# Performance work log

Hardware: AMD Instinct MI355X
Metric: run time of the kernel (lower is better)

The kernel has to match this reference:

```python
import jax, jax.numpy as jnp
import numpy as np

B, N, C, H = 4, 1025, 768, 12
KEEP_RATIO = 0.25
BETA = 1.0


def setup_inputs() -> dict:
    key = jax.random.key(0)
    k1, k2, k3, k4, k5 = jax.random.split(key, 5)
    x = jax.random.normal(k1, (B, N, C), dtype=jnp.float32)
    ucb_count_score = jax.random.uniform(k2, (H, N), dtype=jnp.float32)
    W_qkv = jax.random.normal(k3, (C, 3 * C), dtype=jnp.float32) * 0.02
    W_proj = jax.random.normal(k4, (C, C), dtype=jnp.float32) * 0.02
    b_proj = jax.random.normal(k5, (C,), dtype=jnp.float32) * 0.02
    return {"x": x, "ucb_count_score": ucb_count_score, "W_qkv": W_qkv,
            "W_proj": W_proj, "b_proj": b_proj, "counter": 100, "ucb_enabled": 1}


def reference(x, ucb_count_score, W_qkv, W_proj, b_proj, counter, ucb_enabled):
    Bn, Nn, Cn = x.shape
    Dh = Cn // H
    scale = Dh ** -0.5
    # qkv projection (no bias, qkv_bias=False)
    qkv = (x @ W_qkv).reshape(Bn, Nn, 3, H, Dh)
    q = jnp.transpose(qkv[:, :, 0], (0, 2, 1, 3))  # [B,H,N,Dh]
    k = jnp.transpose(qkv[:, :, 1], (0, 2, 1, 3))
    v = jnp.transpose(qkv[:, :, 2], (0, 2, 1, 3))
    attn_probs = jax.nn.softmax(jnp.einsum('bhnd,bhmd->bhnm', q, k) * scale, axis=-1)

    if ucb_enabled and counter > 50:
        # UCB pruning path (exclude_cls=True, keep_ratio set)
        total_patches = Nn - 1
        k_sel = max(1, int(total_patches * KEEP_RATIO))
        patch_scores = attn_probs[:, :, :, 1:].mean(axis=2)  # [B,H,N-1]
        expl = BETA * jnp.sqrt(jnp.log(counter + 1.0) / (ucb_count_score[:, 1:] + 1e-6))  # [H,N-1]
        global_ucb = (patch_scores + expl[None]).mean(axis=1)  # [B,N-1]
        _, sel = jax.lax.top_k(global_ucb, k_sel)  # [B,k]
        tok = sel + 1  # shift for CLS
        # keep[b,j] = 1 if token j is CLS or selected in batch b
        keep = jnp.zeros((Bn, Nn), dtype=attn_probs.dtype)
        keep = keep.at[jnp.arange(Bn)[:, None], tok].set(1.0).at[:, 0].set(1.0)
        # mask[b,h,i,j] = keep[b,i] OR keep[b,j]
        mask = jnp.maximum(keep[:, None, :, None], keep[:, None, None, :])
        pruned = attn_probs * mask
        pruned = pruned / (pruned.sum(axis=-1, keepdims=True) + 1e-8)
        context = jnp.einsum('bhnm,bhmd->bhnd', pruned, v)
        cnt = jnp.zeros((Nn,), dtype=jnp.float32).at[tok.reshape(-1)].add(1.0) / Bn
        score_delta = jnp.broadcast_to(cnt[None, :], ucb_count_score.shape)
    else:
        context = jnp.einsum('bhnm,bhmd->bhnd', attn_probs, v)
        score_delta = None

    out = context.transpose(0, 2, 1, 3).reshape(Bn, Nn, Cn) @ W_proj + b_proj
    return out, score_delta
```

## Files before the change

### kernel.cpp

```cpp
#include <hip/hip_runtime.h>
#include <hip/hip_bf16.h>
#include <math.h>

#define Bb 4
#define Nn 1025
#define Cc 768
#define Hh 12
#define BH (Bb*Hh)
#define M_ROWS 4100
#define KSEL 256
#define JP 1152
#define IT_TILES 68
#define NIB 17
#define NIB32 33
#define NSW 9
#define MT16 264
#define KC24 24
#define JT16 72
#define JS32 36
#define ESTR 1160
#define NPART 396
#define QSCALE 0.18033688011112042f

#define CAST_X_BLK 1584
#define CAST_WQKV_BLK 864
#define CAST_WPROJ_BLK 288

typedef __attribute__((ext_vector_type(8))) short short8;
typedef __attribute__((ext_vector_type(4))) float floatx4;

static __device__ inline unsigned short f2bf(float v) {
    __hip_bfloat16 b = __float2bfloat16(v);
    return *reinterpret_cast<unsigned short*>(&b);
}
static __device__ inline unsigned short tbf(float f) {
    union { float f; unsigned u; } x; x.f = f;
    return (unsigned short)(x.u >> 16);
}
static __device__ inline float fexp2(float x) {
    return __builtin_amdgcn_exp2f(x);
}
static __device__ inline float bflo(unsigned u) {
    return __uint_as_float((u & 0xffffu) << 16);
}
static __device__ inline float bfhi(unsigned u) {
    return __uint_as_float(u & 0xffff0000u);
}

static __device__ inline void async16(const unsigned short* g, unsigned short* l) {
    __builtin_amdgcn_global_load_lds(
        (const __attribute__((address_space(1))) unsigned int*)g,
        (__attribute__((address_space(3))) unsigned int*)l, 16, 0, 0);
}

__global__ __launch_bounds__(256)
void cast_all(const float* __restrict__ x, const float* __restrict__ Wqkv,
              const float* __restrict__ Wproj,
              unsigned short* __restrict__ xA, unsigned short* __restrict__ WB,
              unsigned short* __restrict__ WpB)
{
    int blk = blockIdx.x;
    int tid = threadIdx.x;
    if (blk < CAST_X_BLK) {
        int s = blk * 256 + tid;
        int ml = s & 15, q = (s >> 4) & 3;
        int t2 = s >> 6;
        int mt = t2 % MT16, kc = t2 / MT16;
        int m = mt * 16 + ml, k = kc * 32 + q * 8;
        uint4 pk = {0u, 0u, 0u, 0u};
        if (m < M_ROWS) {
            float4 a = *(const float4*)&x[(size_t)m * 768 + k];
            float4 b2 = *(const float4*)&x[(size_t)m * 768 + k + 4];
            pk.x = (unsigned)f2bf(a.x)  | ((unsigned)f2bf(a.y)  << 16);
            pk.y = (unsigned)f2bf(a.z)  | ((unsigned)f2bf(a.w)  << 16);
            pk.z = (unsigned)f2bf(b2.x) | ((unsigned)f2bf(b2.y) << 16);
            pk.w = (unsigned)f2bf(b2.z) | ((unsigned)f2bf(b2.w) << 16);
        }
        *(uint4*)&xA[(size_t)s * 8] = pk;
        return;
    }
    const float* W;
    unsigned short* WO;
    int N, NT, s;
    if (blk < CAST_X_BLK + CAST_WQKV_BLK) {
        W = Wqkv; WO = WB; N = 2304; NT = 144;
        s = (blk - CAST_X_BLK) * 256 + tid;
    } else {
        W = Wproj; WO = WpB; N = 768; NT = 48;
        s = (blk - CAST_X_BLK - CAST_WQKV_BLK) * 256 + tid;
    }
    int nl = s & 15, q = (s >> 4) & 3;
    int t2 = s >> 6;
    int nt = t2 % NT, kc = t2 / NT;
    int n = nt * 16 + nl, k = kc * 32 + q * 8;
    unsigned hv[8];
#pragma unroll
    for (int e = 0; e < 8; ++e)
        hv[e] = f2bf(W[(size_t)(k + e) * N + n]);
    uint4 pk;
    pk.x = hv[0] | (hv[1] << 16);
    pk.y = hv[2] | (hv[3] << 16);
    pk.z = hv[4] | (hv[5] << 16);
    pk.w = hv[6] | (hv[7] << 16);
    *(uint4*)&WO[(size_t)s * 8] = pk;
}

__global__ __launch_bounds__(256, 2)
void gemm_mfma(const unsigned short* __restrict__ Af,
               const unsigned short* __restrict__ Bf,
               int Nt16, int mode,
               unsigned short* __restrict__ qB, unsigned short* __restrict__ kF,
               unsigned short* __restrict__ vF,
               float* __restrict__ outp, const float* __restrict__ bias)
{
    __shared__ __align__(16) unsigned short ldsA[4096];
    __shared__ __align__(16) unsigned short ldsB[4096];
    const int tid = threadIdx.x;
    const int ln = tid & 63, w = tid >> 6;
    const int wm = w >> 1, wn = w & 1;
    const int mb = blockIdx.x, nb = blockIdx.y;

    floatx4 acc[4][4];
#pragma unroll
    for (int mt = 0; mt < 4; ++mt)
#pragma unroll
        for (int nt = 0; nt < 4; ++nt)
            acc[mt][nt] = (floatx4){0.f, 0.f, 0.f, 0.f};

    for (int kc = 0; kc < KC24; ++kc) {
        const unsigned short* gA = Af + ((size_t)(kc * MT16 + mb * 8)) * 512;
        const unsigned short* gB = Bf + ((size_t)(kc * Nt16 + nb * 8)) * 512;
        async16(gA + (size_t)(w * 128 + ln) * 8,      &ldsA[w * 1024]);
        async16(gA + (size_t)(w * 128 + 64 + ln) * 8, &ldsA[w * 1024 + 512]);
        async16(gB + (size_t)(w * 128 + ln) * 8,      &ldsB[w * 1024]);
        async16(gB + (size_t)(w * 128 + 64 + ln) * 8, &ldsB[w * 1024 + 512]);
        __syncthreads();

        short8 Am[4], Bn[4];
#pragma unroll
        for (int mt = 0; mt < 4; ++mt)
            Am[mt] = *(const short8*)&ldsA[((wm * 4 + mt) * 64 + ln) * 8];
#pragma unroll
        for (int nt = 0; nt < 4; ++nt)
            Bn[nt] = *(const short8*)&ldsB[((wn * 4 + nt) * 64 + ln) * 8];
#pragma unroll
        for (int mt = 0; mt < 4; ++mt)
#pragma unroll
            for (int nt = 0; nt < 4; ++nt)
                acc[mt][nt] = __builtin_amdgcn_mfma_f32_16x16x32_bf16(
                    Am[mt], Bn[nt], acc[mt][nt], 0, 0, 0);
        __syncthreads();
    }

    const int q = ln >> 4, l15 = ln & 15;
    if (mode == 1) {
#pragma unroll
        for (int nt = 0; nt < 4; ++nt) {
            int gn = nb * 128 + wn * 64 + nt * 16 + l15;
            float bv = bias[gn];
#pragma unroll
            for (int mt = 0; mt < 4; ++mt) {
                int gmb = mb * 128 + wm * 64 + mt * 16 + q * 4;
#pragma unroll
                for (int r = 0; r < 4; ++r) {
                    int gm = gmb + r;
                    if (gm < M_ROWS)
                        outp[(size_t)gm * 768 + gn] = acc[mt][nt][r] + bv;
                }
            }
        }
    } else {
#pragma unroll
        for (int nt = 0; nt < 4; ++nt) {
            int gn = nb * 128 + wn * 64 + nt * 16 + l15;
            int s = (gn >= 1536) ? 2 : (gn >= 768 ? 1 : 0);
            int rr = gn - s * Cc;
            int h = rr >> 6, d = rr & 63;
#pragma unroll
            for (int mt = 0; mt < 4; ++mt) {
                int gmb = mb * 128 + wm * 64 + mt * 16 + q * 4;
#pragma unroll
                for (int r = 0; r < 4; ++r) {
                    int gm = gmb + r;
                    if (gm >= M_ROWS) continue;
                    int b = gm / Nn;
                    int n = gm - b * Nn;
                    int bh = b * Hh + h;
                    float val = acc[mt][nt][r];
                    if (s == 0) {
                        int idx = (((bh * IT_TILES + (n >> 4)) * 2 + (d >> 5)) * 512)
                                  + ((((d & 31) >> 3) * 16 + (n & 15)) * 8) + (d & 7);
                        qB[idx] = f2bf(val * QSCALE);
                    } else if (s == 1) {
                        size_t idx = ((((size_t)bh * JT16 + (n >> 4)) * 2 + (d >> 5)) * 64
                                      + ((d >> 3) & 3) * 16 + (n & 15)) * 8 + (d & 7);
                        kF[idx] = f2bf(val);
                    } else {
                        size_t idx = ((((size_t)bh * JS32 + (n >> 5)) * 4 + (d >> 4)) * 64
                                      + ((n >> 3) & 3) * 16 + (d & 15)) * 8 + (n & 7);
                        vF[idx] = f2bf(val);
                    }
                }
            }
        }
    }
}

__global__ __launch_bounds__(256, 2)
void attn_colsum_mfma(const unsigned short* __restrict__ qB,
                      const unsigned short* __restrict__ kF,
                      float* __restrict__ colsum_part)
{
    __shared__ unsigned short expS[32 * ESTR];
    __shared__ float red16[16][32];
    __shared__ float linv[32];

    const int blk = blockIdx.x;
    const int x8 = blk & 7, g = blk >> 3;
    const int bh = x8 * 6 + (g % 6);
    const int ib = g / 6;
    const int tid = threadIdx.x;
    const int ws = tid >> 6;
    const int ln = tid & 63;
    const int i16 = ln & 15, q = ln >> 4;

    const unsigned short* kBase = kF + (size_t)bh * JT16 * 1024;

    short8 Qf[2][2];
#pragma unroll
    for (int it = 0; it < 2; ++it)
#pragma unroll
        for (int kc = 0; kc < 2; ++kc)
            Qf[it][kc] = *(const short8*)&qB[(((size_t)bh * IT_TILES + ib * 2 + it) * 2 + kc) * 512 + ln * 8];

    float lacc[2][2] = {{0.f, 0.f}, {0.f, 0.f}};

    short8 Kc[2][2], Kn[2][2];
#pragma unroll
    for (int jt = 0; jt < 2; ++jt)
#pragma unroll
        for (int kc = 0; kc < 2; ++kc)
            Kc[jt][kc] = *(const short8*)&kBase[(((ws * 2 + jt) * 2 + kc) * 64 + ln) * 8];

    for (int sw = 0; sw < NSW; ++sw) {
        if (sw + 1 < NSW) {
#pragma unroll
            for (int jt = 0; jt < 2; ++jt)
#pragma unroll
                for (int kc = 0; kc < 2; ++kc)
                    Kn[jt][kc] = *(const short8*)&kBase[((((sw + 1) * 8 + ws * 2 + jt) * 2 + kc) * 64 + ln) * 8];
        }

        floatx4 S[2][2];
#pragma unroll
        for (int it = 0; it < 2; ++it)
#pragma unroll
            for (int jt = 0; jt < 2; ++jt) {
                S[it][jt] = (floatx4){0.f, 0.f, 0.f, 0.f};
#pragma unroll
                for (int kc = 0; kc < 2; ++kc)
                    S[it][jt] = __builtin_amdgcn_mfma_f32_16x16x32_bf16(Kc[jt][kc], Qf[it][kc], S[it][jt], 0, 0, 0);
            }

        const int jbase0 = sw * 128 + ws * 32 + q * 4;
#pragma unroll
        for (int it = 0; it < 2; ++it) {
            const int irow = it * 16 + i16;
#pragma unroll
            for (int jt = 0; jt < 2; ++jt) {
                int jbase = jbase0 + jt * 16;
                float p[4];
#pragma unroll
                for (int r = 0; r < 4; ++r) {
                    float vld = (jbase + r < Nn) ? 1.f : 0.f;
                    p[r] = fexp2(S[it][jt][r]) * vld;
                }
                lacc[it][jt] += (p[0] + p[1]) + (p[2] + p[3]);
                uint2 pk;
                pk.x = (unsigned)tbf(p[0]) | ((unsigned)tbf(p[1]) << 16);
                pk.y = (unsigned)tbf(p[2]) | ((unsigned)tbf(p[3]) << 16);
                *(uint2*)&expS[irow * ESTR + jbase] = pk;
            }
        }
#pragma unroll
        for (int jt = 0; jt < 2; ++jt)
#pragma unroll
            for (int kc = 0; kc < 2; ++kc)
                Kc[jt][kc] = Kn[jt][kc];
    }

    __syncthreads();
#pragma unroll
    for (int it = 0; it < 2; ++it)
        red16[ws * 4 + q][it * 16 + i16] = lacc[it][0] + lacc[it][1];
    __syncthreads();
    if (tid < 32) {
        float s = 0.f;
#pragma unroll
        for (int t = 0; t < 16; ++t) s += red16[t][tid];
        int gi = ib * 32 + tid;
        linv[tid] = (gi < Nn) ? 1.f / s : 0.f;
    }
    __syncthreads();

    float* prow = colsum_part + (size_t)(bh * NIB32 + ib) * JP;
    for (int grp = tid; grp < 288; grp += 256) {
        int j0 = grp * 4;
        float a0 = 0.f, a1 = 0.f, a2 = 0.f, a3 = 0.f;
#pragma unroll 8
        for (int i = 0; i < 32; ++i) {
            uint2 v = *(const uint2*)&expS[i * ESTR + j0];
            float li = linv[i];
            a0 += bflo(v.x) * li;
            a1 += bfhi(v.x) * li;
            a2 += bflo(v.y) * li;
            a3 += bfhi(v.y) * li;
        }
        float4 o = {a0, a1, a2, a3};
        *(float4*)&prow[j0] = o;
    }
}

__global__ __launch_bounds__(1024)
void ucb_topk(const float* __restrict__ colsum_part, const float* __restrict__ ucb_score,
              const int* __restrict__ counter_p,
              float* __restrict__ keepP, float* __restrict__ cnt_b)
{
    const int b = blockIdx.x;
    const int tid = threadIdx.x;
    __shared__ float vals[1024];
    __shared__ int   idxs[1024];

    for (int t = tid; t < JP; t += 1024) {
        keepP[b * JP + t] = 0.f;
        cnt_b[b * JP + t] = 0.f;
    }

    const int j = tid + 1;
    const float* pb = colsum_part + (size_t)b * NPART * JP + j;
    float c0 = 0.f, c1 = 0.f, c2 = 0.f, c3 = 0.f;
#pragma unroll 4
    for (int g2 = 0; g2 < NPART; g2 += 4) {
        c0 += pb[(size_t)(g2 + 0) * JP];
        c1 += pb[(size_t)(g2 + 1) * JP];
        c2 += pb[(size_t)(g2 + 2) * JP];
        c3 += pb[(size_t)(g2 + 3) * JP];
    }
    float cs = (c0 + c1) + (c2 + c3);

    float lc = logf((float)(*counter_p) + 1.0f);
    float s = cs * (1.0f / (float)Nn);
#pragma unroll
    for (int h = 0; h < Hh; ++h)
        s += sqrtf(lc / (ucb_score[h * Nn + j] + 1e-6f));
    s *= (1.0f / (float)Hh);
    vals[tid] = s; idxs[tid] = tid;
    __syncthreads();

    for (int k = 2; k <= 1024; k <<= 1) {
        for (int jj = k >> 1; jj > 0; jj >>= 1) {
            int partner = tid ^ jj;
            if (partner > tid) {
                float v1 = vals[tid], v2 = vals[partner];
                int i1 = idxs[tid], i2 = idxs[partner];
                bool gt = (v1 > v2) || (v1 == v2 && i1 < i2);
                bool desc = ((tid & k) == 0);
                if (desc ? !gt : gt) {
                    vals[tid] = v2; vals[partner] = v1;
                    idxs[tid] = i2; idxs[partner] = i1;
                }
            }
            __syncthreads();
        }
    }

    if (tid < KSEL) {
        int tok = idxs[tid] + 1;
        keepP[b * JP + tok] = 1.f;
        cnt_b[b * JP + tok] = 1.0f / (float)Bb;
    }
    if (tid == 0) keepP[b * JP + 0] = 1.f;
}

__global__ __launch_bounds__(256, 2)
void attn_ctx_mfma(const unsigned short* __restrict__ qB,
                   const unsigned short* __restrict__ kF,
                   const unsigned short* __restrict__ vF,
                   const float* __restrict__ keepP, const float* __restrict__ cnt_b,
                   unsigned short* __restrict__ ctxA, float* __restrict__ out2)
{
    __shared__ __align__(16) char smem[29440];
    unsigned short* Pall = (unsigned short*)smem;
    float* red16 = (float*)(smem + 20480);
    float* dinv  = (float*)(smem + 24576);
    float* keeps = (float*)(smem + 24832);
    float* redC  = (float*)smem;

    const int blk = blockIdx.x;
    const int x8 = blk & 7, g = blk >> 3;
    const int bh = x8 * 6 + (g % 6);
    const int ib = g / 6;
    const int b = bh / Hh, h = bh % Hh;
    const int tid = threadIdx.x;
    const int ws = tid >> 6;
    const int ln = tid & 63;
    const int i16 = ln & 15, q = ln >> 4;

    {
        int t = blk * 256 + tid;
        if (t < Hh * Nn) {
            int n = t % Nn;
            out2[t] = cnt_b[0 * JP + n] + cnt_b[1 * JP + n]
                    + cnt_b[2 * JP + n] + cnt_b[3 * JP + n];
        }
    }

    for (int t = tid; t < JP; t += 256) keeps[t] = keepP[b * JP + t];

    const unsigned short* kBase = kF + (size_t)bh * JT16 * 1024;
    const unsigned short* vBase = vF + (size_t)bh * JS32 * 2048;

    short8 Qf[4][2];
#pragma unroll
    for (int it = 0; it < 4; ++it)
#pragma unroll
        for (int kc = 0; kc < 2; ++kc)
            Qf[it][kc] = *(const short8*)&qB[(((size_t)bh * IT_TILES + ib * 4 + it) * 2 + kc) * 512 + ln * 8];

    __syncthreads();

    float keepi[4];
#pragma unroll
    for (int it = 0; it < 4; ++it)
        keepi[it] = keeps[(ib * 4 + it) * 16 + i16];

    floatx4 ctxacc[4][4];
#pragma unroll
    for (int it = 0; it < 4; ++it)
#pragma unroll
        for (int dt = 0; dt < 4; ++dt)
            ctxacc[it][dt] = (floatx4){0.f, 0.f, 0.f, 0.f};
    float dsacc[4] = {0.f, 0.f, 0.f, 0.f};

    unsigned short* Pw = Pall + ws * 2560;

    short8 Kc[2][2], Kn[2][2], Vc[4], Vn[4];
#pragma unroll
    for (int jt = 0; jt < 2; ++jt)
#pragma unroll
        for (int kc = 0; kc < 2; ++kc)
            Kc[jt][kc] = *(const short8*)&kBase[(((ws * 2 + jt) * 2 + kc) * 64 + ln) * 8];
#pragma unroll
    for (int dt = 0; dt < 4; ++dt)
        Vc[dt] = *(const short8*)&vBase[((ws * 4 + dt) * 64 + ln) * 8];

    for (int sw = 0; sw < NSW; ++sw) {
        if (sw + 1 < NSW) {
#pragma unroll
            for (int jt = 0; jt < 2; ++jt)
#pragma unroll
                for (int kc = 0; kc < 2; ++kc)
                    Kn[jt][kc] = *(const short8*)&kBase[((((sw + 1) * 8 + ws * 2 + jt) * 2 + kc) * 64 + ln) * 8];
#pragma unroll
            for (int dt = 0; dt < 4; ++dt)
                Vn[dt] = *(const short8*)&vBase[((((sw + 1) * 4 + ws) * 4 + dt) * 64 + ln) * 8];
        }

        float kjv[2][4], vld[2][4];
#pragma unroll
        for (int jt = 0; jt < 2; ++jt)
#pragma unroll
            for (int r = 0; r < 4; ++r) {
                int jj = sw * 128 + ws * 32 + jt * 16 + q * 4 + r;
                vld[jt][r] = (jj < Nn) ? 1.f : 0.f;
                kjv[jt][r] = keeps[jj];
            }

#pragma unroll
        for (int it = 0; it < 4; ++it) {
            floatx4 S[2];
#pragma unroll
            for (int jt = 0; jt < 2; ++jt) {
                S[jt] = (floatx4){0.f, 0.f, 0.f, 0.f};
#pragma unroll
                for (int kc = 0; kc < 2; ++kc)
                    S[jt] = __builtin_amdgcn_mfma_f32_16x16x32_bf16(Kc[jt][kc], Qf[it][kc], S[jt], 0, 0, 0);
            }
            bool rk = keepi[it] > 0.5f;
#pragma unroll
            for (int jt = 0; jt < 2; ++jt) {
                float p[4];
#pragma unroll
                for (int r = 0; r < 4; ++r) {
                    float w = rk ? vld[jt][r] : kjv[jt][r];
                    p[r] = fexp2(S[jt][r]) * w;
                    dsacc[it] += p[r];
                }
                unsigned int lo = (unsigned)tbf(p[0]) | ((unsigned)tbf(p[1]) << 16);
                unsigned int hi = (unsigned)tbf(p[2]) | ((unsigned)tbf(p[3]) << 16);
                uint2 pk; pk.x = lo; pk.y = hi;
                *(uint2*)&Pw[(it * 16 + i16) * 40 + jt * 16 + q * 4] = pk;
            }
        }

        short8 Pf[4];
#pragma unroll
        for (int it = 0; it < 4; ++it)
            Pf[it] = *(const short8*)&Pw[(it * 16 + i16) * 40 + q * 8];
#pragma unroll
        for (int it = 0; it < 4; ++it)
#pragma unroll
            for (int dt = 0; dt < 4; ++dt)
                ctxacc[it][dt] = __builtin_amdgcn_mfma_f32_16x16x32_bf16(Pf[it], Vc[dt], ctxacc[it][dt], 0, 0, 0);

#pragma unroll
        for (int jt = 0; jt < 2; ++jt)
#pragma unroll
            for (int kc = 0; kc < 2; ++kc)
                Kc[jt][kc] = Kn[jt][kc];
#pragma unroll
        for (int dt = 0; dt < 4; ++dt)
            Vc[dt] = Vn[dt];
    }

    __syncthreads();
#pragma unroll
    for (int it = 0; it < 4; ++it) red16[(ws * 4 + q) * 64 + it * 16 + i16] = dsacc[it];
    __syncthreads();
    if (tid < 64) {
        float s = 0.f;
#pragma unroll
        for (int t = 0; t < 16; ++t) s += red16[t * 64 + tid];
        dinv[tid] = 1.f / (s + 1e-8f);
    }
    for (int w = 0; w < 4; ++w) {
        __syncthreads();
        if (ws == w) {
#pragma unroll
            for (int it = 0; it < 4; ++it)
#pragma unroll
                for (int dt = 0; dt < 4; ++dt)
#pragma unroll
                    for (int r = 0; r < 4; ++r) {
                        int i = it * 16 + q * 4 + r;
                        int d = dt * 16 + i16;
                        float v = ctxacc[it][dt][r];
                        redC[i * 66 + d] = (w == 0) ? v : (redC[i * 66 + d] + v);
                    }
        }
    }
    __syncthreads();
#pragma unroll
    for (int rep = 0; rep < 2; ++rep) {
        int s2 = tid + rep * 256;
        int i = s2 >> 3, dc = s2 & 7;
        int gi = ib * 64 + i;
        if (gi < Nn) {
            int m = b * Nn + gi;
            float dv = dinv[i];
            const float* src = &redC[i * 66 + dc * 8];
            uint4 pk;
            pk.x = (unsigned)f2bf(src[0] * dv) | ((unsigned)f2bf(src[1] * dv) << 16);
            pk.y = (unsigned)f2bf(src[2] * dv) | ((unsigned)f2bf(src[3] * dv) << 16);
            pk.z = (unsigned)f2bf(src[4] * dv) | ((unsigned)f2bf(src[5] * dv) << 16);
            pk.w = (unsigned)f2bf(src[6] * dv) | ((unsigned)f2bf(src[7] * dv) << 16);
            int kc2 = h * 2 + (dc >> 2);
            int q2 = dc & 3;
            size_t idx = (((size_t)(kc2 * MT16 + (m >> 4))) * 64 + q2 * 16 + (m & 15)) * 8;
            *(uint4*)&ctxA[idx] = pk;
        }
    }
}

extern "C" void kernel_launch(void* const* d_in, const int* in_sizes, int n_in,
                              void* d_out, int out_size, void* d_ws, size_t ws_size,
                              hipStream_t stream) {
    const float* x     = (const float*)d_in[0];
    const float* ucb   = (const float*)d_in[1];
    const float* Wqkv  = (const float*)d_in[2];
    const float* Wproj = (const float*)d_in[3];
    const float* bproj = (const float*)d_in[4];
    const int*   counter = (const int*)d_in[5];

    unsigned short* qB = (unsigned short*)d_ws;
    unsigned short* kF = qB + 3342336;
    unsigned short* vF = kF + 3538944;
    float* keepP    = (float*)(vF + 3538944);
    float* cnt_b    = keepP + 4608;
    unsigned short* ctxA = (unsigned short*)(cnt_b + 4608);
    unsigned short* xA   = ctxA + 3244032;
    unsigned short* WB   = xA + 3244032;
    unsigned short* WpB  = WB + 1769472;
    float* colsum_part = (float*)(WpB + 589824);

    float* out  = (float*)d_out;
    float* out2 = out + 3148800;

    cast_all<<<dim3(CAST_X_BLK + CAST_WQKV_BLK + CAST_WPROJ_BLK), dim3(256), 0, stream>>>(
        x, Wqkv, Wproj, xA, WB, WpB);
    gemm_mfma<<<dim3(33, 18), dim3(256), 0, stream>>>(
        xA, WB, 144, 0, qB, kF, vF, nullptr, nullptr);
    attn_colsum_mfma<<<dim3(8 * 198), dim3(256), 0, stream>>>(qB, kF, colsum_part);
    ucb_topk<<<dim3(Bb), dim3(1024), 0, stream>>>(colsum_part, ucb, counter, keepP, cnt_b);
    attn_ctx_mfma<<<dim3(8 * 102), dim3(256), 0, stream>>>(qB, kF, vF, keepP, cnt_b, ctxA, out2);
    gemm_mfma<<<dim3(33, 6), dim3(256), 0, stream>>>(
        ctxA, WpB, 48, 1, nullptr, nullptr, nullptr, out, bproj);
}
```

Before: 226.3 us.

## Feed P directly from registers into 16x16x16 MFMA, dropping LDS round-trip

Rewrites the V layout into 16-token tiles with 4-element packing so the softmax-probability accumulator output of the S MFMA can be used directly as the A operand of a 16x16x16 bf16 MFMA. This removes the per-iteration LDS write and read of the P tile and shrinks shared memory. The trade is twice as many smaller-K MFMA instructions (16x16x16 instead of 16x16x32) and narrower V loads.

```diff
diff --git a/kernel.cpp b/kernel.cpp
--- a/kernel.cpp
+++ b/kernel.cpp
@@ -17,7 +17,6 @@
 #define MT16 264
 #define KC24 24
 #define JT16 72
-#define JS32 36
 #define ESTR 1160
 #define NPART 396
 #define QSCALE 0.18033688011112042f
@@ -27,11 +26,16 @@
 #define CAST_WPROJ_BLK 288
 
 typedef __attribute__((ext_vector_type(8))) short short8;
+typedef __attribute__((ext_vector_type(4))) short short4s;
 typedef __attribute__((ext_vector_type(4))) float floatx4;
 
 static __device__ inline unsigned short f2bf(float v) {
     __hip_bfloat16 b = __float2bfloat16(v);
     return *reinterpret_cast<unsigned short*>(&b);
+}
+static __device__ inline short tbfs(float f) {
+    union { float f; unsigned u; } x; x.f = f;
+    return (short)(x.u >> 16);
 }
 static __device__ inline unsigned short tbf(float f) {
     union { float f; unsigned u; } x; x.f = f;
@@ -196,8 +200,8 @@
                                       + ((d >> 3) & 3) * 16 + (n & 15)) * 8 + (d & 7);
                         kF[idx] = f2bf(val);
                     } else {
-                        size_t idx = ((((size_t)bh * JS32 + (n >> 5)) * 4 + (d >> 4)) * 64
-                                      + ((n >> 3) & 3) * 16 + (d & 15)) * 8 + (n & 7);
+                        size_t idx = ((((size_t)bh * JT16 + (n >> 4)) * 4 + (d >> 4)) * 64
+                                      + ((n >> 2) & 3) * 16 + (d & 15)) * 4 + (n & 3);
                         vF[idx] = f2bf(val);
                     }
                 }
@@ -389,12 +393,11 @@
                    const float* __restrict__ keepP, const float* __restrict__ cnt_b,
                    unsigned short* __restrict__ ctxA, float* __restrict__ out2)
 {
-    __shared__ __align__(16) char smem[29440];
-    unsigned short* Pall = (unsigned short*)smem;
-    float* red16 = (float*)(smem + 20480);
-    float* dinv  = (float*)(smem + 24576);
-    float* keeps = (float*)(smem + 24832);
-    float* redC  = (float*)smem;
+    __shared__ __align__(16) char smem[25856];
+    float* keeps = (float*)smem;
+    float* red16 = (float*)(smem + 4608);
+    float* dinv  = (float*)(smem + 8704);
+    float* redC  = (float*)(smem + 8960);
 
     const int blk = blockIdx.x;
     const int x8 = blk & 7, g = blk >> 3;
@@ -418,7 +421,7 @@
     for (int t = tid; t < JP; t += 256) keeps[t] = keepP[b * JP + t];
 
     const unsigned short* kBase = kF + (size_t)bh * JT16 * 1024;
-    const unsigned short* vBase = vF + (size_t)bh * JS32 * 2048;
+    const unsigned short* vBase = vF + (size_t)bh * JT16 * 1024;
 
     short8 Qf[4][2];
 #pragma unroll
@@ -442,28 +445,29 @@
             ctxacc[it][dt] = (floatx4){0.f, 0.f, 0.f, 0.f};
     float dsacc[4] = {0.f, 0.f, 0.f, 0.f};
 
-    unsigned short* Pw = Pall + ws * 2560;
-
-    short8 Kc[2][2], Kn[2][2], Vc[4], Vn[4];
-#pragma unroll
-    for (int jt = 0; jt < 2; ++jt)
+    short8 Kc[2][2], Kn[2][2];
+    short4s Vc[2][4], Vn[2][4];
+#pragma unroll
+    for (int jt = 0; jt < 2; ++jt) {
 #pragma unroll
         for (int kc = 0; kc < 2; ++kc)
             Kc[jt][kc] = *(const short8*)&kBase[(((ws * 2 + jt) * 2 + kc) * 64 + ln) * 8];
 #pragma unroll
-    for (int dt = 0; dt < 4; ++dt)
-        Vc[dt] = *(const short8*)&vBase[((ws * 4 + dt) * 64 + ln) * 8];
+        for (int dt = 0; dt < 4; ++dt)
+            Vc[jt][dt] = *(const short4s*)&vBase[(((ws * 2 + jt) * 4 + dt) * 64 + ln) * 4];
+    }
 
     for (int sw = 0; sw < NSW; ++sw) {
         if (sw + 1 < NSW) {
 #pragma unroll
-            for (int jt = 0; jt < 2; ++jt)
+            for (int jt = 0; jt < 2; ++jt) {
 #pragma unroll
                 for (int kc = 0; kc < 2; ++kc)
                     Kn[jt][kc] = *(const short8*)&kBase[((((sw + 1) * 8 + ws * 2 + jt) * 2 + kc) * 64 + ln) * 8];
 #pragma unroll
-            for (int dt = 0; dt < 4; ++dt)
-                Vn[dt] = *(const short8*)&vBase[((((sw + 1) * 4 + ws) * 4 + dt) * 64 + ln) * 8];
+                for (int dt = 0; dt < 4; ++dt)
+                    Vn[jt][dt] = *(const short4s*)&vBase[((((sw + 1) * 8 + ws * 2 + jt) * 4 + dt) * 64 + ln) * 4];
+            }
         }
 
         float kjv[2][4], vld[2][4];
@@ -496,31 +500,25 @@
                     p[r] = fexp2(S[jt][r]) * w;
                     dsacc[it] += p[r];
                 }
-                unsigned int lo = (unsigned)tbf(p[0]) | ((unsigned)tbf(p[1]) << 16);
-                unsigned int hi = (unsigned)tbf(p[2]) | ((unsigned)tbf(p[3]) << 16);
-                uint2 pk; pk.x = lo; pk.y = hi;
-                *(uint2*)&Pw[(it * 16 + i16) * 40 + jt * 16 + q * 4] = pk;
-            }
-        }
-
-        short8 Pf[4];
-#pragma unroll
-        for (int it = 0; it < 4; ++it)
-            Pf[it] = *(const short8*)&Pw[(it * 16 + i16) * 40 + q * 8];
-#pragma unroll
-        for (int it = 0; it < 4; ++it)
-#pragma unroll
-            for (int dt = 0; dt < 4; ++dt)
-                ctxacc[it][dt] = __builtin_amdgcn_mfma_f32_16x16x32_bf16(Pf[it], Vc[dt], ctxacc[it][dt], 0, 0, 0);
-
-#pragma unroll
-        for (int jt = 0; jt < 2; ++jt)
+                short4s Pa;
+                Pa.x = tbfs(p[0]); Pa.y = tbfs(p[1]);
+                Pa.z = tbfs(p[2]); Pa.w = tbfs(p[3]);
+#pragma unroll
+                for (int dt = 0; dt < 4; ++dt)
+                    ctxacc[it][dt] = __builtin_amdgcn_mfma_f32_16x16x16bf16_1k(
+                        Pa, Vc[jt][dt], ctxacc[it][dt], 0, 0, 0);
+            }
+        }
+
+#pragma unroll
+        for (int jt = 0; jt < 2; ++jt) {
 #pragma unroll
             for (int kc = 0; kc < 2; ++kc)
                 Kc[jt][kc] = Kn[jt][kc];
 #pragma unroll
-        for (int dt = 0; dt < 4; ++dt)
-            Vc[dt] = Vn[dt];
+            for (int dt = 0; dt < 4; ++dt)
+                Vc[jt][dt] = Vn[jt][dt];
+        }
     }
 
     __syncthreads();
```

After: 227.4 us. Within noise of the previous version (+0.5%).
